# Optimization experiments

Measured on AMD Instinct MI355X. Metric: run time of the kernel, lower is better.

Reference implementation:

```python
import jax, jax.numpy as jnp
import numpy as np

S = 4096
V = 50000
E = 512
H = 512
CE = 128
CH = 128
T = 50


def _lstm_dir(x, W_ih, W_hh, b, reverse):
    # x: [S, D]; PyTorch gate order i, f, g, o. b = b_ih + b_hh fused.
    gx = x @ W_ih.T + b  # [S, 4H] precomputed input contribution
    Hd = W_hh.shape[1]
    def step(carry, g_t):
        h, c = carry
        g = g_t + h @ W_hh.T
        i, f, gg, o = jnp.split(g, 4, axis=-1)
        c = jax.nn.sigmoid(f) * c + jax.nn.sigmoid(i) * jnp.tanh(gg)
        h = jax.nn.sigmoid(o) * jnp.tanh(c)
        return (h, c), h
    init = (jnp.zeros((Hd,), x.dtype), jnp.zeros((Hd,), x.dtype))
    _, hs = jax.lax.scan(step, init, gx, reverse=reverse)
    return hs  # [S, H]


def _bilstm(x, Wih_f, Whh_f, b_f, Wih_b, Whh_b, b_b):
    fwd = _lstm_dir(x, Wih_f, Whh_f, b_f, False)
    bwd = _lstm_dir(x, Wih_b, Whh_b, b_b, True)
    return jnp.concatenate([fwd, bwd], axis=-1)  # [S, 2H]


def _viterbi(emissions, start_t, end_t, trans):
    # emissions: [S, T]. Standard CRF Viterbi (torchcrf semantics).
    score0 = start_t + emissions[0]  # [T]
    def step(score, emit):
        m = score[:, None] + trans          # [T_prev, T_cur]
        bp = jnp.argmax(m, axis=0)          # best previous tag for each cur tag
        new_score = jnp.max(m, axis=0) + emit
        return new_score, bp
    final, bps = jax.lax.scan(step, score0, emissions[1:])  # bps: [S-1, T]
    final = final + end_t
    last = jnp.argmax(final)
    def back(tag, bp):
        prev = bp[tag]
        return prev, prev
    _, path_head = jax.lax.scan(back, last, bps, reverse=True)  # [S-1]
    return jnp.concatenate([path_head, last[None]])  # [S]


def setup_inputs() -> dict:
    key = jax.random.key(0)
    ks = jax.random.split(key, 20)
    s = 0.05
    inp = {
        'sentence': jax.random.randint(ks[0], (S,), 0, V),
        'char_sentence': jax.random.randint(ks[1], (S,), 0, V),
        'word_emb': jax.random.normal(ks[2], (V, E), jnp.float32) * s,
        'char_emb': jax.random.normal(ks[3], (V, CE), jnp.float32) * s,
        # char BiLSTM
        'cWih_f': jax.random.normal(ks[4], (4 * CH, CE), jnp.float32) * s,
        'cWhh_f': jax.random.normal(ks[5], (4 * CH, CH), jnp.float32) * s,
        'cb_f': jnp.zeros((4 * CH,), jnp.float32),
        'cWih_b': jax.random.normal(ks[6], (4 * CH, CE), jnp.float32) * s,
        'cWhh_b': jax.random.normal(ks[7], (4 * CH, CH), jnp.float32) * s,
        'cb_b': jnp.zeros((4 * CH,), jnp.float32),
        # word BiLSTM (input dim E + 2*CH)
        'wWih_f': jax.random.normal(ks[8], (4 * H, E + 2 * CH), jnp.float32) * s,
        'wWhh_f': jax.random.normal(ks[9], (4 * H, H), jnp.float32) * s,
        'wb_f': jnp.zeros((4 * H,), jnp.float32),
        'wWih_b': jax.random.normal(ks[10], (4 * H, E + 2 * CH), jnp.float32) * s,
        'wWhh_b': jax.random.normal(ks[11], (4 * H, H), jnp.float32) * s,
        'wb_b': jnp.zeros((4 * H,), jnp.float32),
        # hidden2tag
        'W_tag': jax.random.normal(ks[12], (T, 2 * H), jnp.float32) * s,
        'b_tag': jnp.zeros((T,), jnp.float32),
        # CRF params
        'start_t': jax.random.normal(ks[13], (T,), jnp.float32) * s,
        'end_t': jax.random.normal(ks[14], (T,), jnp.float32) * s,
        'trans': jax.random.normal(ks[15], (T, T), jnp.float32) * s,
    }
    return inp


def reference(sentence, char_sentence, word_emb, char_emb,
              cWih_f, cWhh_f, cb_f, cWih_b, cWhh_b, cb_b,
              wWih_f, wWhh_f, wb_f, wWih_b, wWhh_b, wb_b,
              W_tag, b_tag, start_t, end_t, trans):
    we = word_emb[sentence]          # [S, E]
    ce = char_emb[char_sentence]     # [S, CE]
    char_out = _bilstm(ce, cWih_f, cWhh_f, cb_f, cWih_b, cWhh_b, cb_b)  # [S, 2*CH]
    emb = jnp.concatenate([we, char_out], axis=-1)  # [S, E + 2*CH]
    lstm_out = _bilstm(emb, wWih_f, wWhh_f, wb_f, wWih_b, wWhh_b, wb_b)  # [S, 2H]
    tag_space = lstm_out @ W_tag.T + b_tag  # [S, T] emissions
    path = _viterbi(tag_space, start_t, end_t, trans)  # [S] int32 tags
    return path
```

## Files before the change

kernel.cpp:

```cpp
#include <hip/hip_runtime.h>
#include <math.h>

#define SQ   4096
#define EDIM 512
#define CEDIM 128
#define CHH  128
#define WH   512
#define NT   50

typedef unsigned long long ull;

__device__ __forceinline__ float sigf(float x) { return 1.0f / (1.0f + expf(-x)); }

#define PIN4(V) asm volatile("" : "+v"(V.x), "+v"(V.y), "+v"(V.z), "+v"(V.w));

__device__ __forceinline__ void ld8x_sc0(const ull* p, ull& q0, ull& q1, ull& q2,
                                         ull& q3, ull& q4, ull& q5, ull& q6, ull& q7) {
    asm volatile("global_load_dwordx2 %0, %8, off sc0\n\t"
                 "global_load_dwordx2 %1, %8, off offset:8 sc0\n\t"
                 "global_load_dwordx2 %2, %8, off offset:16 sc0\n\t"
                 "global_load_dwordx2 %3, %8, off offset:24 sc0\n\t"
                 "global_load_dwordx2 %4, %8, off offset:32 sc0\n\t"
                 "global_load_dwordx2 %5, %8, off offset:40 sc0\n\t"
                 "global_load_dwordx2 %6, %8, off offset:48 sc0\n\t"
                 "global_load_dwordx2 %7, %8, off offset:56 sc0\n\t"
                 "s_waitcnt vmcnt(0)"
                 : "=&v"(q0), "=&v"(q1), "=&v"(q2), "=&v"(q3),
                   "=&v"(q4), "=&v"(q5), "=&v"(q6), "=&v"(q7)
                 : "v"(p) : "memory");
}
__device__ __forceinline__ void ld2x_sc0(const ull* p, ull& q0, ull& q1) {
    asm volatile("global_load_dwordx2 %0, %2, off sc0\n\t"
                 "global_load_dwordx2 %1, %2, off offset:8 sc0\n\t"
                 "s_waitcnt vmcnt(0)"
                 : "=&v"(q0), "=&v"(q1) : "v"(p) : "memory");
}
__device__ __forceinline__ ull ld_mir(const ull* p) {
    return __hip_atomic_load(p, __ATOMIC_RELAXED, __HIP_MEMORY_SCOPE_AGENT);
}
__device__ __forceinline__ void st_plain8(ull* p, ull v) {
    asm volatile("global_store_dwordx2 %0, %1, off" :: "v"(p), "v"(v) : "memory");
}
__device__ __forceinline__ void st_mir(ull* p, ull v) {
    __hip_atomic_store(p, v, __ATOMIC_RELAXED, __HIP_MEMORY_SCOPE_AGENT);
}
__device__ __forceinline__ unsigned umin2(unsigned a, unsigned b) { return a < b ? a : b; }

#define FMA4(W, off) { float4 h4 = *(const float4*)&hc[off]; \
    a0 += W.x * h4.x; a1 += W.y * h4.y; a2 += W.z * h4.z; a3 += W.w * h4.w; }

__global__ __launch_bounds__(256) void k1_gather_cgx(
    const int* __restrict__ sent, const int* __restrict__ csent,
    const float* __restrict__ wemb, const float* __restrict__ cemb,
    const float* __restrict__ cWih_f, const float* __restrict__ cb_f,
    const float* __restrict__ cWih_b, const float* __restrict__ cb_b,
    float* __restrict__ we_g, float* __restrict__ cgx)
{
    const int tid = threadIdx.x;
    const int t0 = blockIdx.x * 16;
    __shared__ __align__(16) float ceL[16][128];
    __shared__ int sids[16], cids[16];
    if (tid < 16) sids[tid] = sent[t0 + tid];
    else if (tid < 32) cids[tid - 16] = csent[t0 + tid - 16];
    __syncthreads();
    {
        int f4 = tid;
        for (int q = 0; q < 2; ++q, f4 += 256) {
            int r = f4 >> 5, k4 = f4 & 31;
            float4 v = *(const float4*)&cemb[(size_t)cids[r] * CEDIM + k4 * 4];
            *(float4*)&ceL[r][k4 * 4] = v;
        }
    }
    {
        int f4 = tid;
        for (int q = 0; q < 8; ++q, f4 += 256) {
            int r = f4 >> 7, k4 = f4 & 127;
            float4 v = *(const float4*)&wemb[(size_t)sids[r] * EDIM + k4 * 4];
            *(float4*)&we_g[(size_t)(t0 + r) * EDIM + k4 * 4] = v;
        }
    }
    __syncthreads();
    for (int q = 0; q < 4; ++q) {
        int j = q * 256 + tid;
        int d = j >> 9, r = j & 511;
        const float* Wih = d ? cWih_b : cWih_f;
        const float* cb = d ? cb_b : cb_f;
        float b = cb[r];
        float acc[16];
#pragma unroll
        for (int tt = 0; tt < 16; ++tt) acc[tt] = b;
        for (int k4 = 0; k4 < 32; ++k4) {
            float4 wv = *(const float4*)&Wih[r * CEDIM + k4 * 4];
#pragma unroll
            for (int tt = 0; tt < 16; ++tt) {
                acc[tt] += wv.x * ceL[tt][k4 * 4 + 0] + wv.y * ceL[tt][k4 * 4 + 1]
                         + wv.z * ceL[tt][k4 * 4 + 2] + wv.w * ceL[tt][k4 * 4 + 3];
            }
        }
#pragma unroll
        for (int tt = 0; tt < 16; ++tt)
            cgx[((size_t)d * SQ + (t0 + tt)) * 512 + r] = acc[tt];
    }
}

__global__ __launch_bounds__(512, 2) void k2_charlstm_gemm(
    const float* __restrict__ cWhh_f, const float* __restrict__ cWhh_b,
    const float* __restrict__ cgx, float* __restrict__ cho,
    const float* __restrict__ we_g,
    const float* __restrict__ wWih_f, const float* __restrict__ wb_f,
    const float* __restrict__ wWih_b, const float* __restrict__ wb_b,
    float* __restrict__ wgx, ull* __restrict__ pairs)
{
    const int tid = threadIdx.x;
    __shared__ __align__(16) float At[32][68];
    __shared__ __align__(16) float Bt[32][128];
    __shared__ __align__(16) float hstC[128];
    __shared__ float partC[8][65];

    if (blockIdx.x < 64) {
        if ((blockIdx.x & 7) > 1) return;
        const int dir = blockIdx.x & 7;
        const int wid = blockIdx.x >> 3;
        const int k = tid >> 6;
        const int r = tid & 63;
        const int g = r >> 4, u = r & 15;
        const float* Whh = dir ? cWhh_b : cWhh_f;
        const int G = g * CHH + wid * 16 + u;
        const float4* wp = (const float4*)&Whh[(size_t)G * CHH + k * 16];
        float4 w0 = wp[0], w1 = wp[1], w2 = wp[2], w3 = wp[3];
        PIN4(w0) PIN4(w1) PIN4(w2) PIN4(w3)

        ull* cpf = pairs + 4096;
        ull* cpm = pairs + 4608;
        const float* gxc = cgx + (size_t)dir * SQ * 512;
        float cst = 0.f;
        int useFast = 1, alive = 1;
        for (int t = 0; t < SQ; ++t) {
            const int x = dir ? (SQ - 1 - t) : t;
            float gxi = 0.f, gxf = 0.f, gxg = 0.f, gxo = 0.f;
            if (tid < 16) {
                const size_t gb = (size_t)x * 512 + wid * 16 + tid;
                gxi = gxc[gb]; gxf = gxc[gb + 128];
                gxg = gxc[gb + 256]; gxo = gxc[gb + 384];
            }
            if (t == 0) {
                if (tid < 32) *(float4*)&hstC[tid * 4] = make_float4(0, 0, 0, 0);
            } else if (k == 0) {
                const size_t boff = ((size_t)((t - 1) & 1) * 2 + dir) * 128 + tid * 2;
                const ull* pf = cpf + boff;
                const ull* pm = cpm + boff;
                ull q0 = 0, q1 = 0;
                int spins = 0;
                while (alive) {
                    if (useFast) ld2x_sc0(pf, q0, q1);
                    else { q0 = ld_mir(pm + 0); q1 = ld_mir(pm + 1); }
                    unsigned tm = umin2((unsigned)(q0 >> 32), (unsigned)(q1 >> 32));
                    if (__all(tm >= (unsigned)t)) break;
                    ++spins;
                    if (useFast && spins > 2048) { useFast = 0; spins = 0; }
                    if (!useFast && spins > (1 << 20)) alive = 0;
                    __builtin_amdgcn_s_sleep(1);
                }
                hstC[tid * 2 + 0] = __uint_as_float((unsigned)q0);
                hstC[tid * 2 + 1] = __uint_as_float((unsigned)q1);
            }
            __syncthreads();
            float a0 = 0.f, a1 = 0.f, a2 = 0.f, a3 = 0.f;
            const float* hc = &hstC[k * 16];
            FMA4(w0, 0) FMA4(w1, 4) FMA4(w2, 8) FMA4(w3, 12)
            partC[k][r] = (a0 + a1) + (a2 + a3);
            __syncthreads();
            if (tid < 16) {
                float s0 = 0.f, s1 = 0.f, s2 = 0.f, s3 = 0.f;
#pragma unroll
                for (int w8 = 0; w8 < 8; ++w8) {
                    s0 += partC[w8][tid];      s1 += partC[w8][16 + tid];
                    s2 += partC[w8][32 + tid]; s3 += partC[w8][48 + tid];
                }
                float iv = s0 + gxi, fv = s1 + gxf, gv = s2 + gxg, ov = s3 + gxo;
                cst = sigf(fv) * cst + sigf(iv) * tanhf(gv);
                float h = sigf(ov) * tanhf(cst);
                const int unit = wid * 16 + tid;
                cho[(size_t)x * 256 + dir * CHH + unit] = h;
                ull q = ((ull)(unsigned)(t + 1) << 32) | (ull)__float_as_uint(h);
                const size_t poff = ((size_t)(t & 1) * 2 + dir) * 128 + unit;
                st_plain8(cpf + poff, q);
                st_mir(cpm + poff, q);
            }
        }
        return;
    }
    const int tile = blockIdx.x - 64;
    const int dir = tile >> 10;
    const int rem = tile & 1023;
    const int mb = rem >> 4;
    const int nb = rem & 15;
    const float* Wih = dir ? wWih_b : wWih_f;
    const float* wb = dir ? wb_b : wb_f;
    float* C = wgx + (size_t)dir * SQ * 2048;
    const int tm = tid >> 5, tn = tid & 31;
    float acc[4][4];
#pragma unroll
    for (int i = 0; i < 4; ++i)
#pragma unroll
        for (int jj = 0; jj < 4; ++jj) acc[i][jj] = 0.f;
    for (int kb = 0; kb < 16; ++kb) {
        {
            int rowm = tid >> 3, k4 = tid & 7;
            float4 v = *(const float4*)&we_g[(size_t)(mb * 64 + rowm) * EDIM + kb * 32 + k4 * 4];
            At[k4 * 4 + 0][rowm] = v.x; At[k4 * 4 + 1][rowm] = v.y;
            At[k4 * 4 + 2][rowm] = v.z; At[k4 * 4 + 3][rowm] = v.w;
        }
#pragma unroll
        for (int q = 0; q < 2; ++q) {
            int f4 = q * 512 + tid;
            int rr = f4 >> 3, k4 = f4 & 7;
            float4 v = *(const float4*)&Wih[(size_t)(nb * 128 + rr) * 768 + kb * 32 + k4 * 4];
            Bt[k4 * 4 + 0][rr] = v.x; Bt[k4 * 4 + 1][rr] = v.y;
            Bt[k4 * 4 + 2][rr] = v.z; Bt[k4 * 4 + 3][rr] = v.w;
        }
        __syncthreads();
#pragma unroll
        for (int kk = 0; kk < 32; ++kk) {
            float4 a4 = *(const float4*)&At[kk][tm * 4];
            float4 b4 = *(const float4*)&Bt[kk][tn * 4];
            acc[0][0] += a4.x * b4.x; acc[0][1] += a4.x * b4.y; acc[0][2] += a4.x * b4.z; acc[0][3] += a4.x * b4.w;
            acc[1][0] += a4.y * b4.x; acc[1][1] += a4.y * b4.y; acc[1][2] += a4.y * b4.z; acc[1][3] += a4.y * b4.w;
            acc[2][0] += a4.z * b4.x; acc[2][1] += a4.z * b4.y; acc[2][2] += a4.z * b4.z; acc[2][3] += a4.z * b4.w;
            acc[3][0] += a4.w * b4.x; acc[3][1] += a4.w * b4.y; acc[3][2] += a4.w * b4.z; acc[3][3] += a4.w * b4.w;
        }
        __syncthreads();
    }
    float4 wbv = *(const float4*)&wb[nb * 128 + tn * 4];
#pragma unroll
    for (int i = 0; i < 4; ++i) {
        float4 o;
        o.x = acc[i][0] + wbv.x; o.y = acc[i][1] + wbv.y;
        o.z = acc[i][2] + wbv.z; o.w = acc[i][3] + wbv.w;
        *(float4*)&C[(size_t)(mb * 64 + tm * 4 + i) * 2048 + nb * 128 + tn * 4] = o;
    }
}

__global__ __launch_bounds__(512, 2) void k3_gemm_char(
    const float* __restrict__ cho,
    const float* __restrict__ wWih_f, const float* __restrict__ wWih_b,
    float* __restrict__ wgx)
{
    const int tid = threadIdx.x;
    const int tile = blockIdx.x;
    const int dir = tile >> 10;
    const int rem = tile & 1023;
    const int mb = rem >> 4, nb = rem & 15;
    const float* Wih = dir ? wWih_b : wWih_f;
    float* C = wgx + (size_t)dir * SQ * 2048;
    __shared__ __align__(16) float At[32][68];
    __shared__ __align__(16) float Bt[32][128];
    const int tm = tid >> 5, tn = tid & 31;
    float acc[4][4];
#pragma unroll
    for (int i = 0; i < 4; ++i)
#pragma unroll
        for (int jj = 0; jj < 4; ++jj) acc[i][jj] = 0.f;
    for (int kb = 0; kb < 8; ++kb) {
        {
            int rowm = tid >> 3, k4 = tid & 7;
            float4 v = *(const float4*)&cho[(size_t)(mb * 64 + rowm) * 256 + kb * 32 + k4 * 4];
            At[k4 * 4 + 0][rowm] = v.x; At[k4 * 4 + 1][rowm] = v.y;
            At[k4 * 4 + 2][rowm] = v.z; At[k4 * 4 + 3][rowm] = v.w;
        }
#pragma unroll
        for (int q = 0; q < 2; ++q) {
            int f4 = q * 512 + tid;
            int rr = f4 >> 3, k4 = f4 & 7;
            float4 v = *(const float4*)&Wih[(size_t)(nb * 128 + rr) * 768 + 512 + kb * 32 + k4 * 4];
            Bt[k4 * 4 + 0][rr] = v.x; Bt[k4 * 4 + 1][rr] = v.y;
            Bt[k4 * 4 + 2][rr] = v.z; Bt[k4 * 4 + 3][rr] = v.w;
        }
        __syncthreads();
#pragma unroll
        for (int kk = 0; kk < 32; ++kk) {
            float4 a4 = *(const float4*)&At[kk][tm * 4];
            float4 b4 = *(const float4*)&Bt[kk][tn * 4];
            acc[0][0] += a4.x * b4.x; acc[0][1] += a4.x * b4.y; acc[0][2] += a4.x * b4.z; acc[0][3] += a4.x * b4.w;
            acc[1][0] += a4.y * b4.x; acc[1][1] += a4.y * b4.y; acc[1][2] += a4.y * b4.z; acc[1][3] += a4.y * b4.w;
            acc[2][0] += a4.z * b4.x; acc[2][1] += a4.z * b4.y; acc[2][2] += a4.z * b4.z; acc[2][3] += a4.z * b4.w;
            acc[3][0] += a4.w * b4.x; acc[3][1] += a4.w * b4.y; acc[3][2] += a4.w * b4.z; acc[3][3] += a4.w * b4.w;
        }
        __syncthreads();
    }
#pragma unroll
    for (int i = 0; i < 4; ++i) {
        float* cp = &C[(size_t)(mb * 64 + tm * 4 + i) * 2048 + nb * 128 + tn * 4];
        float4 o = *(float4*)cp;
        o.x += acc[i][0]; o.y += acc[i][1]; o.z += acc[i][2]; o.w += acc[i][3];
        *(float4*)cp = o;
    }
}

__global__ __launch_bounds__(1024, 4) void k4_word_lstm(
    const float* __restrict__ wWhh_f, const float* __restrict__ wWhh_b,
    const float* __restrict__ wgx, float* __restrict__ lstm, ull* __restrict__ pairs)
{
    const int res = blockIdx.x & 7;
    if (res > 1) return;
    const int dir = res;
    const int wid = blockIdx.x >> 3;
    const int tid = threadIdx.x;
    const int k = tid >> 6;
    const int r = tid & 63;
    const int g = r >> 4, u = r & 15;
    const float* Whh = dir ? wWhh_b : wWhh_f;
    const int G = g * WH + wid * 16 + u;
    const float4* wp = (const float4*)&Whh[(size_t)G * WH + k * 32];
    float4 w0 = wp[0], w1 = wp[1], w2 = wp[2], w3 = wp[3];
    float4 w4 = wp[4], w5 = wp[5], w6 = wp[6], w7 = wp[7];
    PIN4(w0) PIN4(w1) PIN4(w2) PIN4(w3) PIN4(w4) PIN4(w5) PIN4(w6) PIN4(w7)

    __shared__ __align__(16) float hst[512];
    __shared__ float part[16][65];

    ull* wpf = pairs;
    ull* wpm = pairs + 2048;
    const float* gx = wgx + (size_t)dir * SQ * 2048;
    float cst = 0.f;
    int useFast = 1, alive = 1;
    for (int t = 0; t < SQ; ++t) {
        const int x = dir ? (SQ - 1 - t) : t;
        float gxi = 0.f, gxf = 0.f, gxg = 0.f, gxo = 0.f;
        if (tid < 16) {
            const size_t gb = (size_t)x * 2048 + wid * 16 + tid;
            gxi = gx[gb]; gxf = gx[gb + 512];
            gxg = gx[gb + 1024]; gxo = gx[gb + 1536];
        }
        if (t == 0) {
            if (tid < 128) *(float4*)&hst[tid * 4] = make_float4(0, 0, 0, 0);
        } else if (tid < 64) {
            const size_t boff = ((size_t)((t - 1) & 1) * 2 + dir) * 512 + tid * 8;
            const ull* pf = wpf + boff;
            const ull* pm = wpm + boff;
            ull q0 = 0, q1 = 0, q2 = 0, q3 = 0, q4 = 0, q5 = 0, q6 = 0, q7 = 0;
            int spins = 0;
            while (alive) {
                if (useFast) {
                    ld8x_sc0(pf, q0, q1, q2, q3, q4, q5, q6, q7);
                } else {
                    q0 = ld_mir(pm + 0); q1 = ld_mir(pm + 1);
                    q2 = ld_mir(pm + 2); q3 = ld_mir(pm + 3);
                    q4 = ld_mir(pm + 4); q5 = ld_mir(pm + 5);
                    q6 = ld_mir(pm + 6); q7 = ld_mir(pm + 7);
                }
                unsigned tm = umin2(umin2(umin2((unsigned)(q0 >> 32), (unsigned)(q1 >> 32)),
                                          umin2((unsigned)(q2 >> 32), (unsigned)(q3 >> 32))),
                                    umin2(umin2((unsigned)(q4 >> 32), (unsigned)(q5 >> 32)),
                                          umin2((unsigned)(q6 >> 32), (unsigned)(q7 >> 32))));
                if (__all(tm >= (unsigned)t)) break;
                ++spins;
                if (useFast && spins > 2048) { useFast = 0; spins = 0; }
                if (!useFast && spins > (1 << 20)) alive = 0;
                __builtin_amdgcn_s_sleep(1);
            }
            float* hd = &hst[tid * 8];
            hd[0] = __uint_as_float((unsigned)q0); hd[1] = __uint_as_float((unsigned)q1);
            hd[2] = __uint_as_float((unsigned)q2); hd[3] = __uint_as_float((unsigned)q3);
            hd[4] = __uint_as_float((unsigned)q4); hd[5] = __uint_as_float((unsigned)q5);
            hd[6] = __uint_as_float((unsigned)q6); hd[7] = __uint_as_float((unsigned)q7);
        }
        __syncthreads();
        float a0 = 0.f, a1 = 0.f, a2 = 0.f, a3 = 0.f;
        const float* hc = &hst[k * 32];
        FMA4(w0, 0)  FMA4(w1, 4)  FMA4(w2, 8)  FMA4(w3, 12)
        FMA4(w4, 16) FMA4(w5, 20) FMA4(w6, 24) FMA4(w7, 28)
        part[k][r] = (a0 + a1) + (a2 + a3);
        __syncthreads();
        if (tid < 16) {
            float s0 = 0.f, s1 = 0.f, s2 = 0.f, s3 = 0.f;
#pragma unroll
            for (int kk = 0; kk < 16; ++kk) {
                s0 += part[kk][tid];      s1 += part[kk][16 + tid];
                s2 += part[kk][32 + tid]; s3 += part[kk][48 + tid];
            }
            float iv = s0 + gxi, fv = s1 + gxf, gv = s2 + gxg, ov = s3 + gxo;
            cst = sigf(fv) * cst + sigf(iv) * tanhf(gv);
            float h = sigf(ov) * tanhf(cst);
            const int unit = wid * 16 + tid;
            lstm[(size_t)x * 1024 + dir * WH + unit] = h;
            ull q = ((ull)(unsigned)(t + 1) << 32) | (ull)__float_as_uint(h);
            const size_t poff = ((size_t)(t & 1) * 2 + dir) * 512 + unit;
            st_plain8(wpf + poff, q);
            st_mir(wpm + poff, q);
        }
    }
}

__global__ __launch_bounds__(64) void k5_emis(
    const float* __restrict__ lstm, const float* __restrict__ Wtag,
    const float* __restrict__ btag, float* __restrict__ emis)
{
    const int t = blockIdx.x, tid = threadIdx.x;
    __shared__ __align__(16) float rowL[1024];
#pragma unroll
    for (int q = 0; q < 4; ++q) {
        int f4 = q * 64 + tid;
        *(float4*)&rowL[f4 * 4] = *(const float4*)&lstm[(size_t)t * 1024 + f4 * 4];
    }
    __syncthreads();
    if (tid < NT) {
        float a0 = 0.f, a1 = 0.f, a2 = 0.f, a3 = 0.f;
        const float* wr = Wtag + (size_t)tid * 1024;
        for (int k4 = 0; k4 < 256; ++k4) {
            float4 wv = *(const float4*)&wr[k4 * 4];
            a0 += wv.x * rowL[k4 * 4 + 0];
            a1 += wv.y * rowL[k4 * 4 + 1];
            a2 += wv.z * rowL[k4 * 4 + 2];
            a3 += wv.w * rowL[k4 * 4 + 3];
        }
        emis[(size_t)t * NT + tid] = btag[tid] + (a0 + a1) + (a2 + a3);
    }
}

__global__ __launch_bounds__(256) void k6a_viterbi(
    const float* __restrict__ emis, const float* __restrict__ start_t,
    const float* __restrict__ end_t, const float* __restrict__ trans,
    unsigned char* __restrict__ bpb, int* __restrict__ last)
{
    const int tid = threadIdx.x;
    const int g = tid >> 6, c = tid & 63;
    __shared__ float sc[64];
    __shared__ float pbest[4][64];
    __shared__ int pbp[4][64];
    const int p0 = g * 13;
    float tr[13];
#pragma unroll
    for (int i = 0; i < 13; ++i) {
        int p = p0 + i;
        tr[i] = (c < NT && p < NT) ? trans[p * NT + c] : -1e30f;
    }
    if (tid < 64) sc[tid] = (tid < NT) ? (start_t[tid] + emis[tid]) : -1e30f;
    __syncthreads();
    for (int t = 1; t < SQ; ++t) {
        float best = -1e30f; int bp = 0;
#pragma unroll
        for (int i = 0; i < 13; ++i) {
            float v = sc[p0 + i] + tr[i];
            if (v > best) { best = v; bp = p0 + i; }
        }
        pbest[g][c] = best; pbp[g][c] = bp;
        __syncthreads();
        if (tid < NT) {
            float b = pbest[0][tid]; int bb = pbp[0][tid];
#pragma unroll
            for (int gg = 1; gg < 4; ++gg) {
                float v = pbest[gg][tid];
                if (v > b) { b = v; bb = pbp[gg][tid]; }
            }
            bpb[(size_t)t * NT + tid] = (unsigned char)bb;
            sc[tid] = b + emis[(size_t)t * NT + tid];
        }
        __syncthreads();
    }
    if (tid == 0) {
        float b = -1e30f; int bi = 0;
        for (int cc = 0; cc < NT; ++cc) {
            float v = sc[cc] + end_t[cc];
            if (v > b) { b = v; bi = cc; }
        }
        *last = bi;
    }
}

__global__ __launch_bounds__(64) void k6b_maps(
    const unsigned char* __restrict__ bpb, int* __restrict__ map_)
{
    const int k = blockIdx.x;
    const int e = threadIdx.x;
    if (k == 0 || e >= NT) return;
    int tag = e;
    for (int i = 63; i >= 0; --i) {
        int t = k * 64 + i;
        tag = bpb[(size_t)t * NT + tag];
    }
    map_[k * NT + e] = tag;
}

__global__ __launch_bounds__(64) void k6c_backtrack(
    const unsigned char* __restrict__ bpb, const int* __restrict__ map_,
    const int* __restrict__ last, int* __restrict__ path)
{
    __shared__ int B[64];
    if (threadIdx.x == 0) {
        int tag = *last;
        B[63] = tag;
        for (int k = 63; k >= 1; --k) {
            tag = map_[k * NT + tag];
            B[k - 1] = tag;
        }
    }
    __syncthreads();
    const int k = threadIdx.x;
    int tag = B[k];
    for (int i = 63; i >= 0; --i) {
        int t = k * 64 + i;
        path[t] = tag;
        if (t >= 1) tag = bpb[(size_t)t * NT + tag];
    }
}

extern "C" void kernel_launch(void* const* d_in, const int* in_sizes, int n_in,
                              void* d_out, int out_size, void* d_ws, size_t ws_size,
                              hipStream_t stream)
{
    const int* sent = (const int*)d_in[0];
    const int* csent = (const int*)d_in[1];
    const float* wemb = (const float*)d_in[2];
    const float* cemb = (const float*)d_in[3];
    const float* cWih_f = (const float*)d_in[4];
    const float* cWhh_f = (const float*)d_in[5];
    const float* cb_f = (const float*)d_in[6];
    const float* cWih_b = (const float*)d_in[7];
    const float* cWhh_b = (const float*)d_in[8];
    const float* cb_b = (const float*)d_in[9];
    const float* wWih_f = (const float*)d_in[10];
    const float* wWhh_f = (const float*)d_in[11];
    const float* wb_f = (const float*)d_in[12];
    const float* wWih_b = (const float*)d_in[13];
    const float* wWhh_b = (const float*)d_in[14];
    const float* wb_b = (const float*)d_in[15];
    const float* Wtag = (const float*)d_in[16];
    const float* btag = (const float*)d_in[17];
    const float* start_t = (const float*)d_in[18];
    const float* end_t = (const float*)d_in[19];
    const float* trans = (const float*)d_in[20];
    int* path = (int*)d_out;

    float* ws = (float*)d_ws;
    float* we_g = ws;
    float* cgx  = we_g + (size_t)SQ * EDIM;
    float* cho  = cgx + (size_t)2 * SQ * 512;
    float* wgx  = cho + (size_t)SQ * 256;
    float* lstm = wgx + (size_t)2 * SQ * 2048;
    float* emis = lstm + (size_t)SQ * 1024;
    ull* pairs  = (ull*)(emis + (size_t)SQ * NT);
    int* map_   = (int*)(pairs + 5120);
    int* lastp  = map_ + 64 * NT;
    unsigned char* bpb = (unsigned char*)(lastp + 4);

    (void)hipMemsetAsync(pairs, 0, 5120 * sizeof(ull), stream);

    k1_gather_cgx<<<SQ / 16, 256, 0, stream>>>(sent, csent, wemb, cemb,
                                               cWih_f, cb_f, cWih_b, cb_b, we_g, cgx);
    k2_charlstm_gemm<<<64 + 2048, 512, 0, stream>>>(cWhh_f, cWhh_b, cgx, cho, we_g,
                                                    wWih_f, wb_f, wWih_b, wb_b, wgx, pairs);
    k3_gemm_char<<<2048, 512, 0, stream>>>(cho, wWih_f, wWih_b, wgx);
    k4_word_lstm<<<256, 1024, 0, stream>>>(wWhh_f, wWhh_b, wgx, lstm, pairs);
    k5_emis<<<SQ, 64, 0, stream>>>(lstm, Wtag, btag, emis);
    k6a_viterbi<<<1, 256, 0, stream>>>(emis, start_t, end_t, trans, bpb, lastp);
    k6b_maps<<<64, 64, 0, stream>>>(bpb, map_);
    k6c_backtrack<<<1, 64, 0, stream>>>(bpb, map_, lastp, path);
}
```

Before: 17.07 ms.

## Run char LSTM per direction in one workgroup, parallelize gate activations

After: 14.14 ms. -17.2%, faster.

```diff
diff --git a/kernel.cpp b/kernel.cpp
--- a/kernel.cpp
+++ b/kernel.cpp
@@ -29,12 +29,6 @@
                    "=&v"(q4), "=&v"(q5), "=&v"(q6), "=&v"(q7)
                  : "v"(p) : "memory");
 }
-__device__ __forceinline__ void ld2x_sc0(const ull* p, ull& q0, ull& q1) {
-    asm volatile("global_load_dwordx2 %0, %2, off sc0\n\t"
-                 "global_load_dwordx2 %1, %2, off offset:8 sc0\n\t"
-                 "s_waitcnt vmcnt(0)"
-                 : "=&v"(q0), "=&v"(q1) : "v"(p) : "memory");
-}
 __device__ __forceinline__ ull ld_mir(const ull* p) {
     return __hip_atomic_load(p, __ATOMIC_RELAXED, __HIP_MEMORY_SCOPE_AGENT);
 }
@@ -103,94 +97,70 @@
     }
 }
 
-__global__ __launch_bounds__(512, 2) void k2_charlstm_gemm(
+__global__ __launch_bounds__(1024, 4) void k2_charlstm_gemm(
     const float* __restrict__ cWhh_f, const float* __restrict__ cWhh_b,
     const float* __restrict__ cgx, float* __restrict__ cho,
     const float* __restrict__ we_g,
     const float* __restrict__ wWih_f, const float* __restrict__ wb_f,
     const float* __restrict__ wWih_b, const float* __restrict__ wb_b,
-    float* __restrict__ wgx, ull* __restrict__ pairs)
+    float* __restrict__ wgx)
 {
     const int tid = threadIdx.x;
     __shared__ __align__(16) float At[32][68];
     __shared__ __align__(16) float Bt[32][128];
     __shared__ __align__(16) float hstC[128];
-    __shared__ float partC[8][65];
-
-    if (blockIdx.x < 64) {
-        if ((blockIdx.x & 7) > 1) return;
-        const int dir = blockIdx.x & 7;
-        const int wid = blockIdx.x >> 3;
-        const int k = tid >> 6;
-        const int r = tid & 63;
-        const int g = r >> 4, u = r & 15;
+    __shared__ float partC[2][516];
+    __shared__ float trC[512];
+
+    if (blockIdx.x < 2) {
+        const int dir = blockIdx.x;
         const float* Whh = dir ? cWhh_b : cWhh_f;
-        const int G = g * CHH + wid * 16 + u;
-        const float4* wp = (const float4*)&Whh[(size_t)G * CHH + k * 16];
+        const int row = tid & 511;
+        const int half = tid >> 9;
+        const float4* wp = (const float4*)&Whh[(size_t)row * CHH + half * 64];
         float4 w0 = wp[0], w1 = wp[1], w2 = wp[2], w3 = wp[3];
-        PIN4(w0) PIN4(w1) PIN4(w2) PIN4(w3)
-
-        ull* cpf = pairs + 4096;
-        ull* cpm = pairs + 4608;
+        float4 w4 = wp[4], w5 = wp[5], w6 = wp[6], w7 = wp[7];
+        float4 w8 = wp[8], w9 = wp[9], w10 = wp[10], w11 = wp[11];
+        float4 w12 = wp[12], w13 = wp[13], w14 = wp[14], w15 = wp[15];
+        PIN4(w0) PIN4(w1) PIN4(w2) PIN4(w3) PIN4(w4) PIN4(w5) PIN4(w6) PIN4(w7)
+        PIN4(w8) PIN4(w9) PIN4(w10) PIN4(w11) PIN4(w12) PIN4(w13) PIN4(w14) PIN4(w15)
+
         const float* gxc = cgx + (size_t)dir * SQ * 512;
         float cst = 0.f;
-        int useFast = 1, alive = 1;
+        if (tid < 32) *(float4*)&hstC[tid * 4] = make_float4(0, 0, 0, 0);
+        __syncthreads();
         for (int t = 0; t < SQ; ++t) {
             const int x = dir ? (SQ - 1 - t) : t;
-            float gxi = 0.f, gxf = 0.f, gxg = 0.f, gxo = 0.f;
-            if (tid < 16) {
-                const size_t gb = (size_t)x * 512 + wid * 16 + tid;
-                gxi = gxc[gb]; gxf = gxc[gb + 128];
-                gxg = gxc[gb + 256]; gxo = gxc[gb + 384];
-            }
-            if (t == 0) {
-                if (tid < 32) *(float4*)&hstC[tid * 4] = make_float4(0, 0, 0, 0);
-            } else if (k == 0) {
-                const size_t boff = ((size_t)((t - 1) & 1) * 2 + dir) * 128 + tid * 2;
-                const ull* pf = cpf + boff;
-                const ull* pm = cpm + boff;
-                ull q0 = 0, q1 = 0;
-                int spins = 0;
-                while (alive) {
-                    if (useFast) ld2x_sc0(pf, q0, q1);
-                    else { q0 = ld_mir(pm + 0); q1 = ld_mir(pm + 1); }
-                    unsigned tm = umin2((unsigned)(q0 >> 32), (unsigned)(q1 >> 32));
-                    if (__all(tm >= (unsigned)t)) break;
-                    ++spins;
-                    if (useFast && spins > 2048) { useFast = 0; spins = 0; }
-                    if (!useFast && spins > (1 << 20)) alive = 0;
-                    __builtin_amdgcn_s_sleep(1);
-                }
-                hstC[tid * 2 + 0] = __uint_as_float((unsigned)q0);
-                hstC[tid * 2 + 1] = __uint_as_float((unsigned)q1);
+            float gxv = (tid < 512) ? gxc[(size_t)x * 512 + tid] : 0.f;
+            float a0 = 0.f, a1 = 0.f, a2 = 0.f, a3 = 0.f;
+            const float* hc = &hstC[half * 64];
+            FMA4(w0, 0)   FMA4(w1, 4)   FMA4(w2, 8)   FMA4(w3, 12)
+            FMA4(w4, 16)  FMA4(w5, 20)  FMA4(w6, 24)  FMA4(w7, 28)
+            FMA4(w8, 32)  FMA4(w9, 36)  FMA4(w10, 40) FMA4(w11, 44)
+            FMA4(w12, 48) FMA4(w13, 52) FMA4(w14, 56) FMA4(w15, 60)
+            partC[half][row] = (a0 + a1) + (a2 + a3);
+            __syncthreads();
+            if (tid < 512) {
+                float s = partC[0][tid] + partC[1][tid] + gxv;
+                const bool isg = ((tid >> 7) == 2);
+                float y = sigf(isg ? (s + s) : s);
+                trC[tid] = isg ? (y + y - 1.f) : y;
             }
             __syncthreads();
-            float a0 = 0.f, a1 = 0.f, a2 = 0.f, a3 = 0.f;
-            const float* hc = &hstC[k * 16];
-            FMA4(w0, 0) FMA4(w1, 4) FMA4(w2, 8) FMA4(w3, 12)
-            partC[k][r] = (a0 + a1) + (a2 + a3);
+            if (tid < 128) {
+                float iv = trC[tid], fv = trC[128 + tid];
+                float gv = trC[256 + tid], ov = trC[384 + tid];
+                cst = fv * cst + iv * gv;
+                float ts = sigf(cst + cst);
+                float h = ov * (ts + ts - 1.f);
+                hstC[tid] = h;
+                cho[(size_t)x * 256 + dir * CHH + tid] = h;
+            }
             __syncthreads();
-            if (tid < 16) {
-                float s0 = 0.f, s1 = 0.f, s2 = 0.f, s3 = 0.f;
-#pragma unroll
-                for (int w8 = 0; w8 < 8; ++w8) {
-                    s0 += partC[w8][tid];      s1 += partC[w8][16 + tid];
-                    s2 += partC[w8][32 + tid]; s3 += partC[w8][48 + tid];
-                }
-                float iv = s0 + gxi, fv = s1 + gxf, gv = s2 + gxg, ov = s3 + gxo;
-                cst = sigf(fv) * cst + sigf(iv) * tanhf(gv);
-                float h = sigf(ov) * tanhf(cst);
-                const int unit = wid * 16 + tid;
-                cho[(size_t)x * 256 + dir * CHH + unit] = h;
-                ull q = ((ull)(unsigned)(t + 1) << 32) | (ull)__float_as_uint(h);
-                const size_t poff = ((size_t)(t & 1) * 2 + dir) * 128 + unit;
-                st_plain8(cpf + poff, q);
-                st_mir(cpm + poff, q);
-            }
         }
         return;
     }
-    const int tile = blockIdx.x - 64;
+    const int tile = blockIdx.x - 2;
     const int dir = tile >> 10;
     const int rem = tile & 1023;
     const int mb = rem >> 4;
@@ -198,23 +168,19 @@
     const float* Wih = dir ? wWih_b : wWih_f;
     const float* wb = dir ? wb_b : wb_f;
     float* C = wgx + (size_t)dir * SQ * 2048;
-    const int tm = tid >> 5, tn = tid & 31;
-    float acc[4][4];
-#pragma unroll
-    for (int i = 0; i < 4; ++i)
-#pragma unroll
-        for (int jj = 0; jj < 4; ++jj) acc[i][jj] = 0.f;
+    const int tm = tid >> 6, tn = tid & 63;
+    float acc[4][2];
+#pragma unroll
+    for (int i = 0; i < 4; ++i) { acc[i][0] = 0.f; acc[i][1] = 0.f; }
     for (int kb = 0; kb < 16; ++kb) {
-        {
+        if (tid < 512) {
             int rowm = tid >> 3, k4 = tid & 7;
             float4 v = *(const float4*)&we_g[(size_t)(mb * 64 + rowm) * EDIM + kb * 32 + k4 * 4];
             At[k4 * 4 + 0][rowm] = v.x; At[k4 * 4 + 1][rowm] = v.y;
             At[k4 * 4 + 2][rowm] = v.z; At[k4 * 4 + 3][rowm] = v.w;
         }
-#pragma unroll
-        for (int q = 0; q < 2; ++q) {
-            int f4 = q * 512 + tid;
-            int rr = f4 >> 3, k4 = f4 & 7;
+        {
+            int rr = tid >> 3, k4 = tid & 7;
             float4 v = *(const float4*)&Wih[(size_t)(nb * 128 + rr) * 768 + kb * 32 + k4 * 4];
             Bt[k4 * 4 + 0][rr] = v.x; Bt[k4 * 4 + 1][rr] = v.y;
             Bt[k4 * 4 + 2][rr] = v.z; Bt[k4 * 4 + 3][rr] = v.w;
@@ -223,21 +189,20 @@
 #pragma unroll
         for (int kk = 0; kk < 32; ++kk) {
             float4 a4 = *(const float4*)&At[kk][tm * 4];
-            float4 b4 = *(const float4*)&Bt[kk][tn * 4];
-            acc[0][0] += a4.x * b4.x; acc[0][1] += a4.x * b4.y; acc[0][2] += a4.x * b4.z; acc[0][3] += a4.x * b4.w;
-            acc[1][0] += a4.y * b4.x; acc[1][1] += a4.y * b4.y; acc[1][2] += a4.y * b4.z; acc[1][3] += a4.y * b4.w;
-            acc[2][0] += a4.z * b4.x; acc[2][1] += a4.z * b4.y; acc[2][2] += a4.z * b4.z; acc[2][3] += a4.z * b4.w;
-            acc[3][0] += a4.w * b4.x; acc[3][1] += a4.w * b4.y; acc[3][2] += a4.w * b4.z; acc[3][3] += a4.w * b4.w;
-        }
-        __syncthreads();
-    }
-    float4 wbv = *(const float4*)&wb[nb * 128 + tn * 4];
+            float2 b2 = *(const float2*)&Bt[kk][tn * 2];
+            acc[0][0] += a4.x * b2.x; acc[0][1] += a4.x * b2.y;
+            acc[1][0] += a4.y * b2.x; acc[1][1] += a4.y * b2.y;
+            acc[2][0] += a4.z * b2.x; acc[2][1] += a4.z * b2.y;
+            acc[3][0] += a4.w * b2.x; acc[3][1] += a4.w * b2.y;
+        }
+        __syncthreads();
+    }
+    float2 wbv = *(const float2*)&wb[nb * 128 + tn * 2];
 #pragma unroll
     for (int i = 0; i < 4; ++i) {
-        float4 o;
+        float2 o;
         o.x = acc[i][0] + wbv.x; o.y = acc[i][1] + wbv.y;
-        o.z = acc[i][2] + wbv.z; o.w = acc[i][3] + wbv.w;
-        *(float4*)&C[(size_t)(mb * 64 + tm * 4 + i) * 2048 + nb * 128 + tn * 4] = o;
+        *(float2*)&C[(size_t)(mb * 64 + tm * 4 + i) * 2048 + nb * 128 + tn * 2] = o;
     }
 }
 
@@ -326,12 +291,9 @@
     int useFast = 1, alive = 1;
     for (int t = 0; t < SQ; ++t) {
         const int x = dir ? (SQ - 1 - t) : t;
-        float gxi = 0.f, gxf = 0.f, gxg = 0.f, gxo = 0.f;
-        if (tid < 16) {
-            const size_t gb = (size_t)x * 2048 + wid * 16 + tid;
-            gxi = gx[gb]; gxf = gx[gb + 512];
-            gxg = gx[gb + 1024]; gxo = gx[gb + 1536];
-        }
+        float gxv = 0.f;
+        if (tid < 64)
+            gxv = gx[(size_t)x * 2048 + (size_t)(tid >> 4) * 512 + wid * 16 + (tid & 15)];
         if (t == 0) {
             if (tid < 128) *(float4*)&hst[tid * 4] = make_float4(0, 0, 0, 0);
         } else if (tid < 64) {
@@ -372,22 +334,27 @@
         FMA4(w4, 16) FMA4(w5, 20) FMA4(w6, 24) FMA4(w7, 28)
         part[k][r] = (a0 + a1) + (a2 + a3);
         __syncthreads();
-        if (tid < 16) {
-            float s0 = 0.f, s1 = 0.f, s2 = 0.f, s3 = 0.f;
-#pragma unroll
-            for (int kk = 0; kk < 16; ++kk) {
-                s0 += part[kk][tid];      s1 += part[kk][16 + tid];
-                s2 += part[kk][32 + tid]; s3 += part[kk][48 + tid];
+        if (tid < 64) {
+            float s = gxv;
+#pragma unroll
+            for (int kk = 0; kk < 16; ++kk) s += part[kk][tid];
+            const bool isg = ((tid >> 4) == 2);
+            float y = sigf(isg ? (s + s) : s);
+            float val = isg ? (y + y - 1.f) : y;
+            float fv = __shfl(val, 16 + (tid & 15));
+            float gv = __shfl(val, 32 + (tid & 15));
+            float ov = __shfl(val, 48 + (tid & 15));
+            if (tid < 16) {
+                cst = fv * cst + val * gv;
+                float ts = sigf(cst + cst);
+                float h = ov * (ts + ts - 1.f);
+                const int unit = wid * 16 + tid;
+                lstm[(size_t)x * 1024 + dir * WH + unit] = h;
+                ull q = ((ull)(unsigned)(t + 1) << 32) | (ull)__float_as_uint(h);
+                const size_t poff = ((size_t)(t & 1) * 2 + dir) * 512 + unit;
+                st_plain8(wpf + poff, q);
+                st_mir(wpm + poff, q);
             }
-            float iv = s0 + gxi, fv = s1 + gxf, gv = s2 + gxg, ov = s3 + gxo;
-            cst = sigf(fv) * cst + sigf(iv) * tanhf(gv);
-            float h = sigf(ov) * tanhf(cst);
-            const int unit = wid * 16 + tid;
-            lstm[(size_t)x * 1024 + dir * WH + unit] = h;
-            ull q = ((ull)(unsigned)(t + 1) << 32) | (ull)__float_as_uint(h);
-            const size_t poff = ((size_t)(t & 1) * 2 + dir) * 512 + unit;
-            st_plain8(wpf + poff, q);
-            st_mir(wpm + poff, q);
         }
     }
 }
@@ -548,8 +515,8 @@
 
     k1_gather_cgx<<<SQ / 16, 256, 0, stream>>>(sent, csent, wemb, cemb,
                                                cWih_f, cb_f, cWih_b, cb_b, we_g, cgx);
-    k2_charlstm_gemm<<<64 + 2048, 512, 0, stream>>>(cWhh_f, cWhh_b, cgx, cho, we_g,
-                                                    wWih_f, wb_f, wWih_b, wb_b, wgx, pairs);
+    k2_charlstm_gemm<<<2 + 2048, 1024, 0, stream>>>(cWhh_f, cWhh_b, cgx, cho, we_g,
+                                                    wWih_f, wb_f, wWih_b, wb_b, wgx);
     k3_gemm_char<<<2048, 512, 0, stream>>>(cho, wWih_f, wWih_b, wgx);
     k4_word_lstm<<<256, 1024, 0, stream>>>(wWhh_f, wWhh_b, wgx, lstm, pairs);
     k5_emis<<<SQ, 64, 0, stream>>>(lstm, Wtag, btag, emis);
```
